# Kernel optimization log

Hardware: AMD Instinct MI355X
Metric: run time of the kernel (lower is better)

Reference implementation:

```python
import jax, jax.numpy as jnp
import numpy as np

B, Q, D, T, S = 64, 1024, 256, 64, 3  # batch, queries, hidden_dim, targets/image, max_steps


def _hat(w):
    # (...,3) -> (...,3,3)
    z = jnp.zeros_like(w[..., 0])
    wx, wy, wz = w[..., 0], w[..., 1], w[..., 2]
    return jnp.stack([
        jnp.stack([z, -wz, wy], -1),
        jnp.stack([wz, z, -wx], -1),
        jnp.stack([-wy, wx, z], -1),
    ], -2)


def _vee(W):
    return jnp.stack([W[..., 2, 1] - W[..., 1, 2],
                      W[..., 0, 2] - W[..., 2, 0],
                      W[..., 1, 0] - W[..., 0, 1]], -1) * 0.5


def exp_SO3(omega):
    # Rodrigues: (...,3) -> (...,3,3)
    theta = jnp.clip(jnp.linalg.norm(omega, axis=-1, keepdims=True), 1e-12, None)  # (...,1)
    K = _hat(omega / theta)
    K2 = K @ K
    I = jnp.eye(3, dtype=omega.dtype)
    st = jnp.sin(theta)[..., None]
    ct = jnp.cos(theta)[..., None]
    R = I + st * K + (1.0 - ct) * K2
    Ho = _hat(omega)
    R_small = I + Ho + 0.5 * (Ho @ Ho)
    small = (theta[..., 0] < 1e-5).astype(omega.dtype)[..., None, None]
    return R * (1.0 - small) + R_small * small


def log_SO3(R):
    # (...,3,3) -> (...,3)
    tr = jnp.clip(R[..., 0, 0] + R[..., 1, 1] + R[..., 2, 2], -1.0, 3.0)
    theta = jnp.arccos(jnp.clip((tr - 1.0) * 0.5, -1.0, 1.0))[..., None]  # (...,1)
    W = 0.5 * (R - jnp.swapaxes(R, -1, -2))
    v = _vee(W)
    w = v / jnp.clip(jnp.sin(theta), 1e-12, None) * theta
    small = (theta[..., 0] < 1e-5).astype(R.dtype)[..., None]
    return w * (1.0 - small) + v * small


def _mlp(x, w1, b1, w2, b2):
    # Linear -> ReLU -> Linear -> Sigmoid
    h = jax.nn.relu(x @ w1 + b1)
    return jax.nn.sigmoid(h @ w2 + b2)


def setup_inputs() -> dict:
    key = jax.random.key(0)
    ks = iter(jax.random.split(key, 32))

    def lin(fin, fout):
        bound = 1.0 / np.sqrt(fin)
        kw, kb = jax.random.split(next(ks))
        w = jax.random.uniform(kw, (fin, fout), jnp.float32, -bound, bound)
        b = jax.random.uniform(kb, (fout,), jnp.float32, -bound, bound)
        return w, b

    R_pred = exp_SO3(0.5 * jax.random.normal(next(ks), (B, Q, 3), jnp.float32))
    t_pred = jax.random.normal(next(ks), (B, Q, 3), jnp.float32)
    pred_boxes = jax.random.uniform(next(ks), (B, Q, 4), jnp.float32)
    query_features = jax.random.normal(next(ks), (B, Q, D), jnp.float32)
    tgt_R = exp_SO3(0.5 * jax.random.normal(next(ks), (B, T, 3), jnp.float32))
    tgt_t = jax.random.normal(next(ks), (B, T, 3), jnp.float32)
    tgt_boxes = jax.random.uniform(next(ks), (B, T, 4), jnp.float32)
    tgt_features = jax.random.normal(next(ks), (B, T, D), jnp.float32)

    sp_w1, sp_b1 = lin(D, D // 2); sp_w2, sp_b2 = lin(D // 2, S)
    rw_w1, rw_b1 = lin(D, D // 2); rw_w2, rw_b2 = lin(D // 2, 1)
    tw_w1, tw_b1 = lin(D, D // 2); tw_w2, tw_b2 = lin(D // 2, 1)
    mn_w1, mn_b1 = lin(2 * D, D);  mn_w2, mn_b2 = lin(D, 1)
    global_strength = jnp.float32(0.5)

    return dict(R_pred=R_pred, t_pred=t_pred, pred_boxes=pred_boxes,
                query_features=query_features, tgt_R=tgt_R, tgt_t=tgt_t,
                tgt_boxes=tgt_boxes, tgt_features=tgt_features,
                sp_w1=sp_w1, sp_b1=sp_b1, sp_w2=sp_w2, sp_b2=sp_b2,
                rw_w1=rw_w1, rw_b1=rw_b1, rw_w2=rw_w2, rw_b2=rw_b2,
                tw_w1=tw_w1, tw_b1=tw_b1, tw_w2=tw_w2, tw_b2=tw_b2,
                mn_w1=mn_w1, mn_b1=mn_b1, mn_w2=mn_w2, mn_b2=mn_b2,
                global_strength=global_strength)


def reference(R_pred, t_pred, pred_boxes, query_features, tgt_R, tgt_t,
              tgt_boxes, tgt_features, sp_w1, sp_b1, sp_w2, sp_b2,
              rw_w1, rw_b1, rw_w2, rw_b2, tw_w1, tw_b1, tw_w2, tw_b2,
              mn_w1, mn_b1, mn_w2, mn_b2, global_strength):
    # adaptive per-step scales: (B,S)
    step_scales = _mlp(query_features.mean(axis=1), sp_w1, sp_b1, sp_w2, sp_b2)
    step_scales = step_scales * jnp.clip(global_strength, 0.0, 1.0)
    rot_w = _mlp(query_features, rw_w1, rw_b1, rw_w2, rw_b2)    # (B,Q,1)
    trans_w = _mlp(query_features, tw_w1, tw_b1, tw_w2, tw_b2)  # (B,Q,1)

    # nearest-neighbor matching on box centers
    c_pred = pred_boxes[..., :2]               # (B,Q,2)
    cgt = tgt_boxes[..., :2]                   # (B,T,2)
    d = jnp.sum((c_pred[:, :, None, :] - cgt[:, None, :, :]) ** 2, -1)  # (B,Q,T)
    nn_idx = jnp.argmin(d, axis=-1)            # (B,Q)

    matched_feat = jnp.take_along_axis(tgt_features, nn_idx[..., None], axis=1)  # (B,Q,D)
    combined = jnp.concatenate([query_features, matched_feat], -1)               # (B,Q,2D)
    match_w = _mlp(combined, mn_w1, mn_b1, mn_w2, mn_b2)                          # (B,Q,1)

    Rmatch = jnp.take_along_axis(tgt_R, nn_idx[..., None, None], axis=1)  # (B,Q,3,3)
    tmatch = jnp.take_along_axis(tgt_t, nn_idx[..., None], axis=1)        # (B,Q,3)

    Rb, tb = R_pred, t_pred
    for s in range(S):
        scale = step_scales[:, s][:, None, None]                 # (B,1,1)
        w = log_SO3(jnp.swapaxes(Rb, -1, -2) @ Rmatch)           # (B,Q,3)
        adaptive_w = w * rot_w * match_w * scale
        Rb = Rb @ exp_SO3(adaptive_w)
        tb = tb + (tmatch - tb) * trans_w * match_w * scale
    return Rb, tb
```

## Files before the change

kernel.cpp:

```cpp
#include <hip/hip_runtime.h>

typedef __bf16 bf16;
typedef __bf16 bf16x8 __attribute__((ext_vector_type(8)));
typedef float  f32x4  __attribute__((ext_vector_type(4)));

#define QTOT 1024
#define DD   256

__global__ void k_prep(const float* __restrict__ wr, const float* __restrict__ wt,
                       const float* __restrict__ wm, const float* __restrict__ qf,
                       bf16* __restrict__ pk, float* __restrict__ wsMean2) {
  __shared__ float sPart[8][256];
  int blk = blockIdx.x;
  if (blk < 96) {
    int gid = blk * 256 + threadIdx.x;
    const float* W; int N, nK, idx; bf16* dst;
    if (gid < 4096)      { W = wr; N = 128; nK = 8;  idx = gid;        dst = pk; }
    else if (gid < 8192) { W = wt; N = 128; nK = 8;  idx = gid - 4096; dst = pk + 32768; }
    else                 { W = wm; N = 256; nK = 16; idx = gid - 8192; dst = pk + 65536; }
    int tile = idx >> 6, lane = idx & 63;
    int ni = tile / nK, ki = tile % nK;
    int l15 = lane & 15, quad = lane >> 4;
    int n = ni * 16 + l15;
    int kbase = ki * 32 + quad * 8;
    bf16x8 v;
#pragma unroll
    for (int j = 0; j < 8; ++j) v[j] = (bf16)W[(size_t)(kbase + j) * N + n];
    *(bf16x8*)(dst + (size_t)idx * 8) = v;
  } else {
    int mb = blk - 96;
    int b = mb >> 1, chunk = mb & 1;
    int tid = threadIdx.x;
    int rg = tid >> 5, c8 = tid & 31;
    float acc[8] = {0.f,0.f,0.f,0.f,0.f,0.f,0.f,0.f};
    const float* base = qf + ((size_t)b * QTOT + (size_t)chunk * 512) * DD + c8 * 8;
    for (int it = 0; it < 64; ++it) {
      f32x4 v0 = *(const f32x4*)(base + (size_t)(it * 8 + rg) * DD);
      f32x4 v1 = *(const f32x4*)(base + (size_t)(it * 8 + rg) * DD + 4);
#pragma unroll
      for (int j = 0; j < 4; ++j) { acc[j] += v0[j]; acc[4 + j] += v1[j]; }
    }
#pragma unroll
    for (int j = 0; j < 8; ++j) sPart[rg][c8 * 8 + j] = acc[j];
    __syncthreads();
    float s = 0.f;
#pragma unroll
    for (int g = 0; g < 8; ++g) s += sPart[g][tid];
    wsMean2[mb * 256 + tid] = s;
  }
}

__global__ void k_scales(const float* __restrict__ wsMean2,
                         const float* __restrict__ w1, const float* __restrict__ b1,
                         const float* __restrict__ w2, const float* __restrict__ b2,
                         const float* __restrict__ gs, float* __restrict__ outS) {
  __shared__ float sMean[256];
  __shared__ float sHid[128];
  int b = blockIdx.x, tid = threadIdx.x;
  sMean[tid]       = (wsMean2[(b * 2) * 256 + tid]       + wsMean2[(b * 2 + 1) * 256 + tid])       * (1.f / 1024.f);
  sMean[tid + 128] = (wsMean2[(b * 2) * 256 + tid + 128] + wsMean2[(b * 2 + 1) * 256 + tid + 128]) * (1.f / 1024.f);
  __syncthreads();
  float h = b1[tid];
  for (int d = 0; d < 256; ++d) h += sMean[d] * w1[d * 128 + tid];
  sHid[tid] = fmaxf(h, 0.f);
  __syncthreads();
  if (tid < 3) {
    float o = b2[tid];
    for (int k = 0; k < 128; ++k) o += sHid[k] * w2[k * 3 + tid];
    float g = fminf(fmaxf(gs[0], 0.f), 1.f);
    outS[b * 3 + tid] = g / (1.f + expf(-o));
  }
}

__launch_bounds__(256, 4)
__global__ void k_main(const float* __restrict__ R_pred, const float* __restrict__ t_pred,
                       const float* __restrict__ pred_boxes, const float* __restrict__ qf,
                       const float* __restrict__ tgt_R, const float* __restrict__ tgt_t,
                       const float* __restrict__ tgt_boxes, const float* __restrict__ tgt_f,
                       const float* __restrict__ rw_b1, const float* __restrict__ rw_w2, const float* __restrict__ rw_b2,
                       const float* __restrict__ tw_b1, const float* __restrict__ tw_w2, const float* __restrict__ tw_b2,
                       const float* __restrict__ mn_b1, const float* __restrict__ mn_w2, const float* __restrict__ mn_b2,
                       const bf16* __restrict__ pk, const float* __restrict__ scales,
                       float* __restrict__ out) {
  __shared__ __align__(16) bf16 sQ[64 * 264];
  __shared__ float sRedA[4][64];
  __shared__ float sRedB[4][64];
  __shared__ float sRedM[4][64];
  __shared__ int   sNN[64];

  const int tid = threadIdx.x;
  const int b  = blockIdx.x >> 4;
  const int qb = (blockIdx.x & 15) << 6;

  {
    const float* srcQ = qf + ((size_t)(b * QTOT + qb)) * DD;
#pragma unroll
    for (int it = 0; it < 8; ++it) {
      int idx = tid + it * 256;
      int row = idx >> 5, c8 = idx & 31;
      f32x4 q0 = *(const f32x4*)(srcQ + (size_t)row * DD + c8 * 8);
      f32x4 q1 = *(const f32x4*)(srcQ + (size_t)row * DD + c8 * 8 + 4);
      bf16x8 qv;
#pragma unroll
      for (int j = 0; j < 4; ++j) { qv[j] = (bf16)q0[j]; qv[4 + j] = (bf16)q1[j]; }
      *(bf16x8*)(sQ + row * 264 + c8 * 8) = qv;
    }
  }
  {
    int q = tid >> 2, ch = tid & 3;
    size_t gq = (size_t)(b * QTOT + qb + q);
    float px = pred_boxes[gq * 4 + 0];
    float py = pred_boxes[gq * 4 + 1];
    const float* tb = tgt_boxes + ((size_t)b * 64 + ch * 16) * 4;
    float best = 3.4e38f; int bi = ch * 16;
    for (int i = 0; i < 16; ++i) {
      f32x4 bx = *(const f32x4*)(tb + (size_t)i * 4);
      float dx = px - bx[0], dy = py - bx[1];
      float d = __fadd_rn(__fmul_rn(dx, dx), __fmul_rn(dy, dy));
      if (d < best) { best = d; bi = ch * 16 + i; }
    }
#pragma unroll
    for (int m = 1; m < 4; m <<= 1) {
      float pv = __shfl_xor(best, m);
      int   pi = __shfl_xor(bi, m);
      if (pv < best || (pv == best && pi < bi)) { best = pv; bi = pi; }
    }
    if ((tid & 3) == 0) sNN[q] = bi;
  }
  __syncthreads();

  const int lane = tid & 63, wv = tid >> 6;
  const int l15 = lane & 15, quad = lane >> 4;
  const int koff = quad * 8;
  const bf16x8* pRot   = (const bf16x8*)pk;
  const bf16x8* pTrans = (const bf16x8*)(pk + 32768);
  const bf16x8* pMatch = (const bf16x8*)(pk + 65536);

  f32x4 accR[4][2], accT[4][2];
#pragma unroll
  for (int mt = 0; mt < 4; ++mt)
#pragma unroll
    for (int nl = 0; nl < 2; ++nl) {
      accR[mt][nl] = f32x4{0.f, 0.f, 0.f, 0.f};
      accT[mt][nl] = f32x4{0.f, 0.f, 0.f, 0.f};
    }
#pragma unroll
  for (int ks = 0; ks < 8; ++ks) {
    bf16x8 A[4];
#pragma unroll
    for (int mt = 0; mt < 4; ++mt)
      A[mt] = *(const bf16x8*)(sQ + (mt * 16 + l15) * 264 + ks * 32 + koff);
#pragma unroll
    for (int nl = 0; nl < 2; ++nl) {
      bf16x8 Br = pRot[((size_t)((2 * wv + nl) * 8 + ks)) * 64 + lane];
      bf16x8 Bt = pTrans[((size_t)((2 * wv + nl) * 8 + ks)) * 64 + lane];
#pragma unroll
      for (int mt = 0; mt < 4; ++mt) {
        accR[mt][nl] = __builtin_amdgcn_mfma_f32_16x16x32_bf16(A[mt], Br, accR[mt][nl], 0, 0, 0);
        accT[mt][nl] = __builtin_amdgcn_mfma_f32_16x16x32_bf16(A[mt], Bt, accT[mt][nl], 0, 0, 0);
      }
    }
  }
  {
    float b1r[2], w2r[2], b1t[2], w2t[2];
#pragma unroll
    for (int nl = 0; nl < 2; ++nl) {
      int n = (2 * wv + nl) * 16 + l15;
      b1r[nl] = rw_b1[n]; w2r[nl] = rw_w2[n];
      b1t[nl] = tw_b1[n]; w2t[nl] = tw_w2[n];
    }
#pragma unroll
    for (int mt = 0; mt < 4; ++mt)
#pragma unroll
      for (int i = 0; i < 4; ++i) {
        float pr = 0.f, pt = 0.f;
#pragma unroll
        for (int nl = 0; nl < 2; ++nl) {
          pr += fmaxf(accR[mt][nl][i] + b1r[nl], 0.f) * w2r[nl];
          pt += fmaxf(accT[mt][nl][i] + b1t[nl], 0.f) * w2t[nl];
        }
        pr += __shfl_xor(pr, 1); pr += __shfl_xor(pr, 2); pr += __shfl_xor(pr, 4); pr += __shfl_xor(pr, 8);
        pt += __shfl_xor(pt, 1); pt += __shfl_xor(pt, 2); pt += __shfl_xor(pt, 4); pt += __shfl_xor(pt, 8);
        if (l15 == 0) {
          int q = mt * 16 + quad * 4 + i;
          sRedA[wv][q] = pr; sRedB[wv][q] = pt;
        }
      }
  }
  __syncthreads();

  float rw, tw;
  {
    int q = wv * 16 + l15;
    float vr = sRedA[0][q] + sRedA[1][q] + sRedA[2][q] + sRedA[3][q] + rw_b2[0];
    float vt = sRedB[0][q] + sRedB[1][q] + sRedB[2][q] + sRedB[3][q] + tw_b2[0];
    rw = 1.f / (1.f + expf(-vr));
    tw = 1.f / (1.f + expf(-vt));
  }

  f32x4 accM[4][4];
#pragma unroll
  for (int mt = 0; mt < 4; ++mt)
#pragma unroll
    for (int nl = 0; nl < 4; ++nl) accM[mt][nl] = f32x4{0.f, 0.f, 0.f, 0.f};
  int grow[4];
#pragma unroll
  for (int mt = 0; mt < 4; ++mt) grow[mt] = sNN[mt * 16 + l15];
#pragma unroll
  for (int ks = 0; ks < 8; ++ks) {
    bf16x8 A[4];
#pragma unroll
    for (int mt = 0; mt < 4; ++mt)
      A[mt] = *(const bf16x8*)(sQ + (mt * 16 + l15) * 264 + ks * 32 + koff);
#pragma unroll
    for (int nl = 0; nl < 4; ++nl) {
      bf16x8 Bm = pMatch[((size_t)((4 * wv + nl) * 16 + ks)) * 64 + lane];
#pragma unroll
      for (int mt = 0; mt < 4; ++mt)
        accM[mt][nl] = __builtin_amdgcn_mfma_f32_16x16x32_bf16(A[mt], Bm, accM[mt][nl], 0, 0, 0);
    }
  }
#pragma unroll
  for (int ks = 0; ks < 8; ++ks) {
    bf16x8 A[4];
#pragma unroll
    for (int mt = 0; mt < 4; ++mt) {
      const float* src = tgt_f + ((size_t)(b * 64 + grow[mt])) * DD + ks * 32 + koff;
      f32x4 a0 = *(const f32x4*)src;
      f32x4 a1 = *(const f32x4*)(src + 4);
#pragma unroll
      for (int j = 0; j < 4; ++j) { A[mt][j] = (bf16)a0[j]; A[mt][4 + j] = (bf16)a1[j]; }
    }
#pragma unroll
    for (int nl = 0; nl < 4; ++nl) {
      bf16x8 Bm = pMatch[((size_t)((4 * wv + nl) * 16 + 8 + ks)) * 64 + lane];
#pragma unroll
      for (int mt = 0; mt < 4; ++mt)
        accM[mt][nl] = __builtin_amdgcn_mfma_f32_16x16x32_bf16(A[mt], Bm, accM[mt][nl], 0, 0, 0);
    }
  }
  {
    float b1m[4], w2m[4];
#pragma unroll
    for (int nl = 0; nl < 4; ++nl) {
      int n = (4 * wv + nl) * 16 + l15;
      b1m[nl] = mn_b1[n]; w2m[nl] = mn_w2[n];
    }
#pragma unroll
    for (int mt = 0; mt < 4; ++mt)
#pragma unroll
      for (int i = 0; i < 4; ++i) {
        float pm = 0.f;
#pragma unroll
        for (int nl = 0; nl < 4; ++nl) pm += fmaxf(accM[mt][nl][i] + b1m[nl], 0.f) * w2m[nl];
        pm += __shfl_xor(pm, 1); pm += __shfl_xor(pm, 2); pm += __shfl_xor(pm, 4); pm += __shfl_xor(pm, 8);
        if (l15 == 0) sRedM[wv][mt * 16 + quad * 4 + i] = pm;
      }
  }
  __syncthreads();

  if (quad == 0) {
    int q = wv * 16 + l15;
    float vm = sRedM[0][q] + sRedM[1][q] + sRedM[2][q] + sRedM[3][q] + mn_b2[0];
    float mw = 1.f / (1.f + expf(-vm));
    size_t gq = (size_t)(b * QTOT + qb + q);
    float R[9], Rm[9], t[3], tm[3];
#pragma unroll
    for (int i = 0; i < 9; ++i) R[i] = R_pred[gq * 9 + i];
#pragma unroll
    for (int c = 0; c < 3; ++c) t[c] = t_pred[gq * 3 + c];
    size_t gt = (size_t)b * 64 + sNN[q];
#pragma unroll
    for (int i = 0; i < 9; ++i) Rm[i] = tgt_R[gt * 9 + i];
#pragma unroll
    for (int c = 0; c < 3; ++c) tm[c] = tgt_t[gt * 3 + c];

    for (int s = 0; s < 3; ++s) {
      float sc = scales[b * 3 + s];
      float cr = rw * mw * sc, ctr = tw * mw * sc;
      float Ax[9];
#pragma unroll
      for (int i = 0; i < 3; ++i)
#pragma unroll
        for (int j = 0; j < 3; ++j)
          Ax[i * 3 + j] = R[0 + i] * Rm[0 + j] + R[3 + i] * Rm[3 + j] + R[6 + i] * Rm[6 + j];
      float tr = fminf(fmaxf(Ax[0] + Ax[4] + Ax[8], -1.f), 3.f);
      float cthe = fminf(fmaxf((tr - 1.f) * 0.5f, -1.f), 1.f);
      float th = acosf(cthe);
      float vx = 0.5f * (Ax[7] - Ax[5]);
      float vy = 0.5f * (Ax[2] - Ax[6]);
      float vz = 0.5f * (Ax[3] - Ax[1]);
      float f = (th < 1e-5f) ? 1.f : th / fmaxf(sinf(th), 1e-12f);
      float ax = vx * f * cr, ay = vy * f * cr, az = vz * f * cr;
      float th2 = ax * ax + ay * ay + az * az;
      float thn = sqrtf(th2);
      float E[9];
      if (thn < 1e-5f) {
        E[0] = 1.f + 0.5f * (ax * ax - th2); E[1] = -az + 0.5f * ax * ay;        E[2] =  ay + 0.5f * ax * az;
        E[3] =  az + 0.5f * ax * ay;         E[4] = 1.f + 0.5f * (ay * ay - th2); E[5] = -ax + 0.5f * ay * az;
        E[6] = -ay + 0.5f * ax * az;         E[7] =  ax + 0.5f * ay * az;         E[8] = 1.f + 0.5f * (az * az - th2);
      } else {
        float kx = ax / thn, ky = ay / thn, kz = az / thn;
        float st = sinf(thn), co = cosf(thn), c1 = 1.f - co;
        E[0] = co + c1 * kx * kx;      E[1] = c1 * kx * ky - st * kz; E[2] = c1 * kx * kz + st * ky;
        E[3] = c1 * kx * ky + st * kz; E[4] = co + c1 * ky * ky;      E[5] = c1 * ky * kz - st * kx;
        E[6] = c1 * kx * kz - st * ky; E[7] = c1 * ky * kz + st * kx; E[8] = co + c1 * kz * kz;
      }
      float Rn[9];
#pragma unroll
      for (int i = 0; i < 3; ++i)
#pragma unroll
        for (int j = 0; j < 3; ++j)
          Rn[i * 3 + j] = R[i * 3 + 0] * E[j] + R[i * 3 + 1] * E[3 + j] + R[i * 3 + 2] * E[6 + j];
#pragma unroll
      for (int i = 0; i < 9; ++i) R[i] = Rn[i];
#pragma unroll
      for (int c = 0; c < 3; ++c) t[c] += (tm[c] - t[c]) * ctr;
    }
#pragma unroll
    for (int i = 0; i < 9; ++i) out[gq * 9 + i] = R[i];
#pragma unroll
    for (int c = 0; c < 3; ++c) out[(size_t)589824 + gq * 3 + c] = t[c];
  }
}

extern "C" void kernel_launch(void* const* d_in, const int* in_sizes, int n_in,
                              void* d_out, int out_size, void* d_ws, size_t ws_size,
                              hipStream_t stream) {
  const float* R_pred     = (const float*)d_in[0];
  const float* t_pred     = (const float*)d_in[1];
  const float* pred_boxes = (const float*)d_in[2];
  const float* qf         = (const float*)d_in[3];
  const float* tgt_R      = (const float*)d_in[4];
  const float* tgt_t      = (const float*)d_in[5];
  const float* tgt_boxes  = (const float*)d_in[6];
  const float* tgt_f      = (const float*)d_in[7];
  const float* sp_w1 = (const float*)d_in[8];
  const float* sp_b1 = (const float*)d_in[9];
  const float* sp_w2 = (const float*)d_in[10];
  const float* sp_b2 = (const float*)d_in[11];
  const float* rw_w1 = (const float*)d_in[12];
  const float* rw_b1 = (const float*)d_in[13];
  const float* rw_w2 = (const float*)d_in[14];
  const float* rw_b2 = (const float*)d_in[15];
  const float* tw_w1 = (const float*)d_in[16];
  const float* tw_b1 = (const float*)d_in[17];
  const float* tw_w2 = (const float*)d_in[18];
  const float* tw_b2 = (const float*)d_in[19];
  const float* mn_w1 = (const float*)d_in[20];
  const float* mn_b1 = (const float*)d_in[21];
  const float* mn_w2 = (const float*)d_in[22];
  const float* mn_b2 = (const float*)d_in[23];
  const float* gs    = (const float*)d_in[24];

  float* wsScales = (float*)d_ws;
  float* wsMean2  = (float*)((char*)d_ws + 1024);
  bf16*  pk       = (bf16*)((char*)d_ws + 1024 + 131072);
  float* out      = (float*)d_out;

  k_prep<<<224, 256, 0, stream>>>(rw_w1, tw_w1, mn_w1, qf, pk, wsMean2);
  k_scales<<<64, 128, 0, stream>>>(wsMean2, sp_w1, sp_b1, sp_w2, sp_b2, gs, wsScales);
  k_main<<<1024, 256, 0, stream>>>(R_pred, t_pred, pred_boxes, qf, tgt_R, tgt_t, tgt_boxes, tgt_f,
                                   rw_b1, rw_w2, rw_b2, tw_b1, tw_w2, tw_b2, mn_b1, mn_w2, mn_b2,
                                   pk, wsScales, out);
}
```

Before: 237.3 us.

## Precompute target-feature half of match MLP per target instead of per query

Uses linearity of the first match-MLP layer. The target-feature projection (tgt_f @ W1_bottom) is now computed once per target (64 per batch) in a new middle kernel and stored as bf16. k_main then gathers the projected row per matched query instead of running the second K-half of the GEMM on gathered features. This halves the match-MLP MFMA work in the main kernel. It also splits the rot/trans accumulators into separate scopes to lower register pressure, and parallelises the scale-MLP reduction. The cost is an extra bf16 rounding of the projection plus scattered global bf16 gathers.

```diff
diff --git a/kernel.cpp b/kernel.cpp
--- a/kernel.cpp
+++ b/kernel.cpp
@@ -34,6 +34,7 @@
     int rg = tid >> 5, c8 = tid & 31;
     float acc[8] = {0.f,0.f,0.f,0.f,0.f,0.f,0.f,0.f};
     const float* base = qf + ((size_t)b * QTOT + (size_t)chunk * 512) * DD + c8 * 8;
+#pragma unroll 4
     for (int it = 0; it < 64; ++it) {
       f32x4 v0 = *(const f32x4*)(base + (size_t)(it * 8 + rg) * DD);
       f32x4 v1 = *(const f32x4*)(base + (size_t)(it * 8 + rg) * DD + 4);
@@ -50,25 +51,87 @@
   }
 }
 
-__global__ void k_scales(const float* __restrict__ wsMean2,
-                         const float* __restrict__ w1, const float* __restrict__ b1,
-                         const float* __restrict__ w2, const float* __restrict__ b2,
-                         const float* __restrict__ gs, float* __restrict__ outS) {
+__global__ void k_mid(const float* __restrict__ tgt_f, const bf16* __restrict__ pk,
+                      const float* __restrict__ wsMean2,
+                      const float* __restrict__ w1, const float* __restrict__ b1,
+                      const float* __restrict__ w2, const float* __restrict__ b2,
+                      const float* __restrict__ gs,
+                      bf16* __restrict__ tgtp, float* __restrict__ outS) {
+  __shared__ __align__(16) bf16 sT[64 * 264];
   __shared__ float sMean[256];
+  __shared__ float sPart2[256];
   __shared__ float sHid[128];
-  int b = blockIdx.x, tid = threadIdx.x;
-  sMean[tid]       = (wsMean2[(b * 2) * 256 + tid]       + wsMean2[(b * 2 + 1) * 256 + tid])       * (1.f / 1024.f);
-  sMean[tid + 128] = (wsMean2[(b * 2) * 256 + tid + 128] + wsMean2[(b * 2 + 1) * 256 + tid + 128]) * (1.f / 1024.f);
-  __syncthreads();
-  float h = b1[tid];
-  for (int d = 0; d < 256; ++d) h += sMean[d] * w1[d * 128 + tid];
-  sHid[tid] = fmaxf(h, 0.f);
-  __syncthreads();
-  if (tid < 3) {
-    float o = b2[tid];
-    for (int k = 0; k < 128; ++k) o += sHid[k] * w2[k * 3 + tid];
-    float g = fminf(fmaxf(gs[0], 0.f), 1.f);
-    outS[b * 3 + tid] = g / (1.f + expf(-o));
+  int blk = blockIdx.x, tid = threadIdx.x;
+  if (blk < 64) {
+    int b = blk;
+    const float* srcT = tgt_f + ((size_t)b * 64) * DD;
+#pragma unroll
+    for (int it = 0; it < 8; ++it) {
+      int idx = tid + it * 256;
+      int row = idx >> 5, c8 = idx & 31;
+      f32x4 t0 = *(const f32x4*)(srcT + (size_t)row * DD + c8 * 8);
+      f32x4 t1 = *(const f32x4*)(srcT + (size_t)row * DD + c8 * 8 + 4);
+      bf16x8 tv;
+#pragma unroll
+      for (int j = 0; j < 4; ++j) { tv[j] = (bf16)t0[j]; tv[4 + j] = (bf16)t1[j]; }
+      *(bf16x8*)(sT + row * 264 + c8 * 8) = tv;
+    }
+    __syncthreads();
+    const int lane = tid & 63, wv = tid >> 6;
+    const int l15 = lane & 15, quad = lane >> 4, koff = quad * 8;
+    const bf16x8* pMatch = (const bf16x8*)(pk + 65536);
+    f32x4 acc[4][4];
+#pragma unroll
+    for (int mt = 0; mt < 4; ++mt)
+#pragma unroll
+      for (int nl = 0; nl < 4; ++nl) acc[mt][nl] = f32x4{0.f, 0.f, 0.f, 0.f};
+#pragma unroll
+    for (int ks = 0; ks < 8; ++ks) {
+      bf16x8 A[4];
+#pragma unroll
+      for (int mt = 0; mt < 4; ++mt)
+        A[mt] = *(const bf16x8*)(sT + (mt * 16 + l15) * 264 + ks * 32 + koff);
+#pragma unroll
+      for (int nl = 0; nl < 4; ++nl) {
+        bf16x8 Bm = pMatch[((size_t)((4 * wv + nl) * 16 + 8 + ks)) * 64 + lane];
+#pragma unroll
+        for (int mt = 0; mt < 4; ++mt)
+          acc[mt][nl] = __builtin_amdgcn_mfma_f32_16x16x32_bf16(A[mt], Bm, acc[mt][nl], 0, 0, 0);
+      }
+    }
+    bf16* dst = tgtp + (size_t)b * 64 * 256;
+#pragma unroll
+    for (int mt = 0; mt < 4; ++mt)
+#pragma unroll
+      for (int nl = 0; nl < 4; ++nl) {
+        int n = (4 * wv + nl) * 16 + l15;
+#pragma unroll
+        for (int i = 0; i < 4; ++i) {
+          int t = mt * 16 + quad * 4 + i;
+          dst[t * 256 + n] = (bf16)acc[mt][nl][i];
+        }
+      }
+  } else {
+    int b = blk - 64;
+    sMean[tid] = (wsMean2[(2 * b) * 256 + tid] + wsMean2[(2 * b + 1) * 256 + tid]) * (1.f / 1024.f);
+    __syncthreads();
+    int hid = tid & 127, half = tid >> 7;
+    float ph = 0.f;
+#pragma unroll 8
+    for (int dd = 0; dd < 128; ++dd) {
+      int d = half * 128 + dd;
+      ph += sMean[d] * w1[d * 128 + hid];
+    }
+    sPart2[tid] = ph;
+    __syncthreads();
+    if (tid < 128) sHid[tid] = fmaxf(sPart2[tid] + sPart2[tid + 128] + b1[tid], 0.f);
+    __syncthreads();
+    if (tid < 3) {
+      float o = b2[tid];
+      for (int k = 0; k < 128; ++k) o += sHid[k] * w2[k * 3 + tid];
+      float g = fminf(fmaxf(gs[0], 0.f), 1.f);
+      outS[b * 3 + tid] = g / (1.f + expf(-o));
+    }
   }
 }
 
@@ -76,12 +139,12 @@
 __global__ void k_main(const float* __restrict__ R_pred, const float* __restrict__ t_pred,
                        const float* __restrict__ pred_boxes, const float* __restrict__ qf,
                        const float* __restrict__ tgt_R, const float* __restrict__ tgt_t,
-                       const float* __restrict__ tgt_boxes, const float* __restrict__ tgt_f,
+                       const float* __restrict__ tgt_boxes,
                        const float* __restrict__ rw_b1, const float* __restrict__ rw_w2, const float* __restrict__ rw_b2,
                        const float* __restrict__ tw_b1, const float* __restrict__ tw_w2, const float* __restrict__ tw_b2,
                        const float* __restrict__ mn_b1, const float* __restrict__ mn_w2, const float* __restrict__ mn_b2,
-                       const bf16* __restrict__ pk, const float* __restrict__ scales,
-                       float* __restrict__ out) {
+                       const bf16* __restrict__ pk, const bf16* __restrict__ tgtp,
+                       const float* __restrict__ scales, float* __restrict__ out) {
   __shared__ __align__(16) bf16 sQ[64 * 264];
   __shared__ float sRedA[4][64];
   __shared__ float sRedB[4][64];
@@ -136,55 +199,78 @@
   const bf16x8* pTrans = (const bf16x8*)(pk + 32768);
   const bf16x8* pMatch = (const bf16x8*)(pk + 65536);
 
-  f32x4 accR[4][2], accT[4][2];
-#pragma unroll
-  for (int mt = 0; mt < 4; ++mt)
-#pragma unroll
-    for (int nl = 0; nl < 2; ++nl) {
-      accR[mt][nl] = f32x4{0.f, 0.f, 0.f, 0.f};
-      accT[mt][nl] = f32x4{0.f, 0.f, 0.f, 0.f};
-    }
-#pragma unroll
-  for (int ks = 0; ks < 8; ++ks) {
-    bf16x8 A[4];
-#pragma unroll
-    for (int mt = 0; mt < 4; ++mt)
-      A[mt] = *(const bf16x8*)(sQ + (mt * 16 + l15) * 264 + ks * 32 + koff);
-#pragma unroll
-    for (int nl = 0; nl < 2; ++nl) {
-      bf16x8 Br = pRot[((size_t)((2 * wv + nl) * 8 + ks)) * 64 + lane];
-      bf16x8 Bt = pTrans[((size_t)((2 * wv + nl) * 8 + ks)) * 64 + lane];
-#pragma unroll
-      for (int mt = 0; mt < 4; ++mt) {
-        accR[mt][nl] = __builtin_amdgcn_mfma_f32_16x16x32_bf16(A[mt], Br, accR[mt][nl], 0, 0, 0);
-        accT[mt][nl] = __builtin_amdgcn_mfma_f32_16x16x32_bf16(A[mt], Bt, accT[mt][nl], 0, 0, 0);
-      }
-    }
-  }
-  {
-    float b1r[2], w2r[2], b1t[2], w2t[2];
+  {
+    f32x4 accR[4][2];
+#pragma unroll
+    for (int mt = 0; mt < 4; ++mt)
+#pragma unroll
+      for (int nl = 0; nl < 2; ++nl) accR[mt][nl] = f32x4{0.f, 0.f, 0.f, 0.f};
+#pragma unroll
+    for (int ks = 0; ks < 8; ++ks) {
+      bf16x8 A[4];
+#pragma unroll
+      for (int mt = 0; mt < 4; ++mt)
+        A[mt] = *(const bf16x8*)(sQ + (mt * 16 + l15) * 264 + ks * 32 + koff);
+#pragma unroll
+      for (int nl = 0; nl < 2; ++nl) {
+        bf16x8 Br = pRot[((size_t)((2 * wv + nl) * 8 + ks)) * 64 + lane];
+#pragma unroll
+        for (int mt = 0; mt < 4; ++mt)
+          accR[mt][nl] = __builtin_amdgcn_mfma_f32_16x16x32_bf16(A[mt], Br, accR[mt][nl], 0, 0, 0);
+      }
+    }
+    float b1r[2], w2r[2];
 #pragma unroll
     for (int nl = 0; nl < 2; ++nl) {
       int n = (2 * wv + nl) * 16 + l15;
       b1r[nl] = rw_b1[n]; w2r[nl] = rw_w2[n];
+    }
+#pragma unroll
+    for (int mt = 0; mt < 4; ++mt)
+#pragma unroll
+      for (int i = 0; i < 4; ++i) {
+        float pr = 0.f;
+#pragma unroll
+        for (int nl = 0; nl < 2; ++nl) pr += fmaxf(accR[mt][nl][i] + b1r[nl], 0.f) * w2r[nl];
+        pr += __shfl_xor(pr, 1); pr += __shfl_xor(pr, 2); pr += __shfl_xor(pr, 4); pr += __shfl_xor(pr, 8);
+        if (l15 == 0) sRedA[wv][mt * 16 + quad * 4 + i] = pr;
+      }
+  }
+  {
+    f32x4 accT[4][2];
+#pragma unroll
+    for (int mt = 0; mt < 4; ++mt)
+#pragma unroll
+      for (int nl = 0; nl < 2; ++nl) accT[mt][nl] = f32x4{0.f, 0.f, 0.f, 0.f};
+#pragma unroll
+    for (int ks = 0; ks < 8; ++ks) {
+      bf16x8 A[4];
+#pragma unroll
+      for (int mt = 0; mt < 4; ++mt)
+        A[mt] = *(const bf16x8*)(sQ + (mt * 16 + l15) * 264 + ks * 32 + koff);
+#pragma unroll
+      for (int nl = 0; nl < 2; ++nl) {
+        bf16x8 Bt = pTrans[((size_t)((2 * wv + nl) * 8 + ks)) * 64 + lane];
+#pragma unroll
+        for (int mt = 0; mt < 4; ++mt)
+          accT[mt][nl] = __builtin_amdgcn_mfma_f32_16x16x32_bf16(A[mt], Bt, accT[mt][nl], 0, 0, 0);
+      }
+    }
+    float b1t[2], w2t[2];
+#pragma unroll
+    for (int nl = 0; nl < 2; ++nl) {
+      int n = (2 * wv + nl) * 16 + l15;
       b1t[nl] = tw_b1[n]; w2t[nl] = tw_w2[n];
     }
 #pragma unroll
     for (int mt = 0; mt < 4; ++mt)
 #pragma unroll
       for (int i = 0; i < 4; ++i) {
-        float pr = 0.f, pt = 0.f;
-#pragma unroll
-        for (int nl = 0; nl < 2; ++nl) {
-          pr += fmaxf(accR[mt][nl][i] + b1r[nl], 0.f) * w2r[nl];
-          pt += fmaxf(accT[mt][nl][i] + b1t[nl], 0.f) * w2t[nl];
-        }
-        pr += __shfl_xor(pr, 1); pr += __shfl_xor(pr, 2); pr += __shfl_xor(pr, 4); pr += __shfl_xor(pr, 8);
+        float pt = 0.f;
+#pragma unroll
+        for (int nl = 0; nl < 2; ++nl) pt += fmaxf(accT[mt][nl][i] + b1t[nl], 0.f) * w2t[nl];
         pt += __shfl_xor(pt, 1); pt += __shfl_xor(pt, 2); pt += __shfl_xor(pt, 4); pt += __shfl_xor(pt, 8);
-        if (l15 == 0) {
-          int q = mt * 16 + quad * 4 + i;
-          sRedA[wv][q] = pr; sRedB[wv][q] = pt;
-        }
+        if (l15 == 0) sRedB[wv][mt * 16 + quad * 4 + i] = pt;
       }
   }
   __syncthreads();
@@ -198,61 +284,45 @@
     tw = 1.f / (1.f + expf(-vt));
   }
 
-  f32x4 accM[4][4];
-#pragma unroll
-  for (int mt = 0; mt < 4; ++mt)
-#pragma unroll
-    for (int nl = 0; nl < 4; ++nl) accM[mt][nl] = f32x4{0.f, 0.f, 0.f, 0.f};
-  int grow[4];
-#pragma unroll
-  for (int mt = 0; mt < 4; ++mt) grow[mt] = sNN[mt * 16 + l15];
-#pragma unroll
-  for (int ks = 0; ks < 8; ++ks) {
-    bf16x8 A[4];
-#pragma unroll
-    for (int mt = 0; mt < 4; ++mt)
-      A[mt] = *(const bf16x8*)(sQ + (mt * 16 + l15) * 264 + ks * 32 + koff);
-#pragma unroll
-    for (int nl = 0; nl < 4; ++nl) {
-      bf16x8 Bm = pMatch[((size_t)((4 * wv + nl) * 16 + ks)) * 64 + lane];
+  {
+    f32x4 accM[4][4];
+#pragma unroll
+    for (int mt = 0; mt < 4; ++mt)
+#pragma unroll
+      for (int nl = 0; nl < 4; ++nl) accM[mt][nl] = f32x4{0.f, 0.f, 0.f, 0.f};
+#pragma unroll
+    for (int ks = 0; ks < 8; ++ks) {
+      bf16x8 A[4];
 #pragma unroll
       for (int mt = 0; mt < 4; ++mt)
-        accM[mt][nl] = __builtin_amdgcn_mfma_f32_16x16x32_bf16(A[mt], Bm, accM[mt][nl], 0, 0, 0);
-    }
-  }
-#pragma unroll
-  for (int ks = 0; ks < 8; ++ks) {
-    bf16x8 A[4];
-#pragma unroll
-    for (int mt = 0; mt < 4; ++mt) {
-      const float* src = tgt_f + ((size_t)(b * 64 + grow[mt])) * DD + ks * 32 + koff;
-      f32x4 a0 = *(const f32x4*)src;
-      f32x4 a1 = *(const f32x4*)(src + 4);
-#pragma unroll
-      for (int j = 0; j < 4; ++j) { A[mt][j] = (bf16)a0[j]; A[mt][4 + j] = (bf16)a1[j]; }
-    }
-#pragma unroll
-    for (int nl = 0; nl < 4; ++nl) {
-      bf16x8 Bm = pMatch[((size_t)((4 * wv + nl) * 16 + 8 + ks)) * 64 + lane];
-#pragma unroll
-      for (int mt = 0; mt < 4; ++mt)
-        accM[mt][nl] = __builtin_amdgcn_mfma_f32_16x16x32_bf16(A[mt], Bm, accM[mt][nl], 0, 0, 0);
-    }
-  }
-  {
+        A[mt] = *(const bf16x8*)(sQ + (mt * 16 + l15) * 264 + ks * 32 + koff);
+#pragma unroll
+      for (int nl = 0; nl < 4; ++nl) {
+        bf16x8 Bm = pMatch[((size_t)((4 * wv + nl) * 16 + ks)) * 64 + lane];
+#pragma unroll
+        for (int mt = 0; mt < 4; ++mt)
+          accM[mt][nl] = __builtin_amdgcn_mfma_f32_16x16x32_bf16(A[mt], Bm, accM[mt][nl], 0, 0, 0);
+      }
+    }
     float b1m[4], w2m[4];
 #pragma unroll
     for (int nl = 0; nl < 4; ++nl) {
       int n = (4 * wv + nl) * 16 + l15;
       b1m[nl] = mn_b1[n]; w2m[nl] = mn_w2[n];
     }
+    const bf16* tpb = tgtp + (size_t)b * 64 * 256;
 #pragma unroll
     for (int mt = 0; mt < 4; ++mt)
 #pragma unroll
       for (int i = 0; i < 4; ++i) {
+        int nnq = sNN[mt * 16 + quad * 4 + i];
+        const bf16* tprow = tpb + (size_t)nnq * 256;
         float pm = 0.f;
 #pragma unroll
-        for (int nl = 0; nl < 4; ++nl) pm += fmaxf(accM[mt][nl][i] + b1m[nl], 0.f) * w2m[nl];
+        for (int nl = 0; nl < 4; ++nl) {
+          float tp = (float)tprow[(4 * wv + nl) * 16 + l15];
+          pm += fmaxf(accM[mt][nl][i] + b1m[nl] + tp, 0.f) * w2m[nl];
+        }
         pm += __shfl_xor(pm, 1); pm += __shfl_xor(pm, 2); pm += __shfl_xor(pm, 4); pm += __shfl_xor(pm, 8);
         if (l15 == 0) sRedM[wv][mt * 16 + quad * 4 + i] = pm;
       }
@@ -356,11 +426,12 @@
   float* wsScales = (float*)d_ws;
   float* wsMean2  = (float*)((char*)d_ws + 1024);
   bf16*  pk       = (bf16*)((char*)d_ws + 1024 + 131072);
+  bf16*  tgtp     = (bf16*)((char*)d_ws + 1024 + 131072 + 393216);
   float* out      = (float*)d_out;
 
   k_prep<<<224, 256, 0, stream>>>(rw_w1, tw_w1, mn_w1, qf, pk, wsMean2);
-  k_scales<<<64, 128, 0, stream>>>(wsMean2, sp_w1, sp_b1, sp_w2, sp_b2, gs, wsScales);
-  k_main<<<1024, 256, 0, stream>>>(R_pred, t_pred, pred_boxes, qf, tgt_R, tgt_t, tgt_boxes, tgt_f,
+  k_mid<<<128, 256, 0, stream>>>(tgt_f, pk, wsMean2, sp_w1, sp_b1, sp_w2, sp_b2, gs, tgtp, wsScales);
+  k_main<<<1024, 256, 0, stream>>>(R_pred, t_pred, pred_boxes, qf, tgt_R, tgt_t, tgt_boxes,
                                    rw_b1, rw_w2, rw_b2, tw_b1, tw_w2, tw_b2, mn_b1, mn_w2, mn_b2,
-                                   pk, wsScales, out);
+                                   pk, tgtp, wsScales, out);
 }
```

Result: faster. 212.5 us (-10.5%).
